# Optimization experiments

Measured on AMD Instinct MI355X. Metric: run time of the kernel, lower is better.

Reference implementation:

```python
import jax, jax.numpy as jnp
import numpy as np

N = 50000
E = 800000
IN_DIM = 256
H1, D1 = 4, 128   # layer1: 4 heads x 128 = 512 concat
H2, D2 = 1, 256   # layer2: 1 head x 256
NEG_SLOPE = 0.2


def setup_inputs() -> dict:
    key = jax.random.key(0)
    ks = jax.random.split(key, 12)
    feat = jax.random.normal(ks[0], (N, IN_DIM), dtype=jnp.float32)
    src1 = jax.random.randint(ks[1], (E,), 0, N)
    dst1 = jax.random.randint(ks[2], (E,), 0, N)
    src2 = jax.random.randint(ks[3], (E,), 0, N)
    dst2 = jax.random.randint(ks[4], (E,), 0, N)
    s1 = 1.0 / np.sqrt(IN_DIM)
    s2 = 1.0 / np.sqrt(H1 * D1)
    W1 = jax.random.normal(ks[5], (IN_DIM, H1 * D1), dtype=jnp.float32) * s1
    al1 = jax.random.normal(ks[6], (H1, D1), dtype=jnp.float32) * s1
    ar1 = jax.random.normal(ks[7], (H1, D1), dtype=jnp.float32) * s1
    W2 = jax.random.normal(ks[8], (H1 * D1, H2 * D2), dtype=jnp.float32) * s2
    al2 = jax.random.normal(ks[9], (H2, D2), dtype=jnp.float32) * s2
    ar2 = jax.random.normal(ks[10], (H2, D2), dtype=jnp.float32) * s2
    return {"feat": feat, "src1": src1, "dst1": dst1, "src2": src2,
            "dst2": dst2, "W1": W1, "al1": al1, "ar1": ar1,
            "W2": W2, "al2": al2, "ar2": ar2}


def gat_layer(x, W, al, ar, src, dst, heads):
    n = x.shape[0]
    h = (x @ W).reshape(n, heads, -1)               # [N,H,D]
    el = jnp.einsum('nhd,hd->nh', h, al)            # attention left term
    er = jnp.einsum('nhd,hd->nh', h, ar)            # attention right term
    e = jax.nn.leaky_relu(el[src] + er[dst], NEG_SLOPE)   # [E,H]
    # segment softmax over edges grouped by destination node
    m = jax.ops.segment_max(e, dst, num_segments=n)
    m = jax.lax.stop_gradient(jnp.where(jnp.isfinite(m), m, 0.0))
    ee = jnp.exp(e - m[dst])
    s = jax.ops.segment_sum(ee, dst, num_segments=n)
    alpha = ee / (s[dst] + 1e-9)                    # [E,H]
    msg = h[src] * alpha[:, :, None]                # [E,H,D]
    return jax.ops.segment_sum(msg, dst, num_segments=n)  # [N,H,D]


def reference(feat, src1, dst1, src2, dst2, W1, al1, ar1, W2, al2, ar2):
    h1 = gat_layer(feat, W1, al1, ar1, src1, dst1, H1)      # [N,4,128]
    h1 = jax.nn.elu(h1.reshape(N, H1 * D1))                 # concat heads + act
    z = gat_layer(h1, W2, al2, ar2, src2, dst2, H2)         # [N,1,256]
    return z.reshape(N, D2)                                 # no act on last layer
```

## Files before the change

kernel.cpp:

```cpp
#include <hip/hip_runtime.h>
#include <stdint.h>

#define NN 50000
#define EE 800000
#define IND 256
#define HD1 512
#define D2C 256

#define NB1 782
#define NB  (2 * NB1)
#define CH  16384
#define WGN ((2 * EE + CH - 1) / CH)
#define TOT (NB * WGN)
#define SB2 ((TOT + 255) / 256)

#define Q_SCALE 21.166666f
#define Q_INV   0.047244094f

typedef float f32x4 __attribute__((ext_vector_type(4)));
typedef __bf16 bf16x8 __attribute__((ext_vector_type(8)));

__device__ inline float bf2f(unsigned int u) {
    union { unsigned int i; float f; } c; c.i = u << 16; return c.f;
}
__device__ inline unsigned int f2bf(float f) {
    union { float f; unsigned int i; } c; c.f = f;
    unsigned int x = c.i;
    return (x + 0x7FFFu + ((x >> 16) & 1u)) >> 16;
}
__device__ inline float loadf(const void* p, int idx, int isbf) {
    return isbf ? bf2f(((const unsigned short*)p)[idx]) : ((const float*)p)[idx];
}
__device__ inline unsigned int f2q8(float v) {
    float t = fminf(fmaxf(v * Q_SCALE, -127.f), 127.f);
    int q = (int)rintf(t);
    return (unsigned int)q & 0xFFu;
}
__device__ inline void unpack8_q8(uint2 q, float* o) {
    o[0] = (float)(int)(signed char)(q.x & 0xFFu);
    o[1] = (float)(int)(signed char)((q.x >> 8) & 0xFFu);
    o[2] = (float)(int)(signed char)((q.x >> 16) & 0xFFu);
    o[3] = (float)(int)(signed char)(q.x >> 24);
    o[4] = (float)(int)(signed char)(q.y & 0xFFu);
    o[5] = (float)(int)(signed char)((q.y >> 8) & 0xFFu);
    o[6] = (float)(int)(signed char)((q.y >> 16) & 0xFFu);
    o[7] = (float)(int)(signed char)(q.y >> 24);
}
__device__ inline void glds16(const unsigned short* g, unsigned short* lds_base) {
    __builtin_amdgcn_global_load_lds(
        (const __attribute__((address_space(1))) void*)g,
        (__attribute__((address_space(3))) void*)lds_base, 16, 0, 0);
}

__global__ void probe_k(const unsigned int* __restrict__ w, int* __restrict__ flag) {
    __shared__ int red[256];
    int t = threadIdx.x;
    int ok = 0;
    for (int i = t; i < 4096; i += 256) {
        unsigned int v = w[i];
        unsigned int e0 = (v >> 7) & 0xffu;
        unsigned int e1 = (v >> 23) & 0xffu;
        ok += (e0 <= 133u) + (e1 <= 133u);
    }
    red[t] = ok;
    __syncthreads();
    for (int s = 128; s > 0; s >>= 1) {
        if (t < s) red[t] += red[t + s];
        __syncthreads();
    }
    if (t == 0) *flag = (red[0] >= 7782) ? 1 : 0;
}

__global__ __launch_bounds__(256) void convert_k(
    const void* __restrict__ in, const int* __restrict__ flagp,
    unsigned short* __restrict__ out)
{
    int isbf = (*flagp != 0);
    size_t i = ((size_t)blockIdx.x * 256 + threadIdx.x) * 8;
    if (i >= (size_t)NN * IND) return;
    if (isbf) {
        *(uint4*)(out + i) = *(const uint4*)((const unsigned short*)in + i);
    } else {
        const float* f = (const float*)in + i;
        f32x4 p0 = *(const f32x4*)f;
        f32x4 p1 = *(const f32x4*)(f + 4);
        uint4 va;
        va.x = f2bf(p0.x) | (f2bf(p0.y) << 16);
        va.y = f2bf(p0.z) | (f2bf(p0.w) << 16);
        va.z = f2bf(p1.x) | (f2bf(p1.y) << 16);
        va.w = f2bf(p1.z) | (f2bf(p1.w) << 16);
        *(uint4*)(out + i) = va;
    }
}

__global__ __launch_bounds__(256) void gemm_bt(
    const unsigned short* __restrict__ A, const int* __restrict__ flagp,
    const unsigned short* __restrict__ BT,
    void* __restrict__ C, int c_q8,
    int M, int K, int Nc,
    const void* __restrict__ al, const void* __restrict__ ar,
    float* __restrict__ el, float* __restrict__ er, int eler_mode)
{
    __shared__ unsigned short Als[128 * 32];
    __shared__ unsigned short Bls[128 * 32];
    __shared__ float elp[128];
    __shared__ float erp[128];
    int isbf = (*flagp != 0);
    int tid  = threadIdx.x;
    int wave = tid >> 6;
    int lane = tid & 63;
    int wr = (wave >> 1) * 64;
    int wc = (wave & 1) * 64;
    int m0 = blockIdx.x * 128;
    int n0 = blockIdx.y * 128;
    if (tid < 128) { elp[tid] = 0.f; erp[tid] = 0.f; }
    f32x4 acc[4][4];
#pragma unroll
    for (int i = 0; i < 4; i++)
#pragma unroll
        for (int j = 0; j < 4; j++) acc[i][j] = (f32x4){0.f, 0.f, 0.f, 0.f};
    int frow = lane & 15;
    int kg = (lane >> 4) * 8;
    int srow = lane >> 2;
    int scol = (lane & 3) * 8;
    for (int kt = 0; kt < K; kt += 32) {
#pragma unroll
        for (int q = 0; q < 2; ++q) {
            int chunk = wave + q * 4;
            int r = chunk * 16 + srow;
            int gm = m0 + r; if (gm >= M) gm = M - 1;
            glds16(A + (size_t)gm * K + kt + scol, Als + chunk * 512);
            glds16(BT + (size_t)(n0 + r) * K + kt + scol, Bls + chunk * 512);
        }
        __syncthreads();
        bf16x8 af[4], bfr[4];
#pragma unroll
        for (int i = 0; i < 4; i++)
            af[i] = __builtin_bit_cast(bf16x8, *(const uint4*)(Als + (wr + i * 16 + frow) * 32 + kg));
#pragma unroll
        for (int j = 0; j < 4; j++)
            bfr[j] = __builtin_bit_cast(bf16x8, *(const uint4*)(Bls + (wc + j * 16 + frow) * 32 + kg));
#pragma unroll
        for (int i = 0; i < 4; i++)
#pragma unroll
            for (int j = 0; j < 4; j++)
                acc[i][j] = __builtin_amdgcn_mfma_f32_16x16x32_bf16(af[i], bfr[j], acc[i][j], 0, 0, 0);
        __syncthreads();
    }
    int nb = n0 + wc + frow;
    int mb = m0 + wr + (lane >> 4) * 4;
#pragma unroll
    for (int i = 0; i < 4; i++) {
#pragma unroll
        for (int j = 0; j < 4; j++) {
            int n = nb + j * 16;
#pragma unroll
            for (int r = 0; r < 4; r++) {
                int m = mb + i * 16 + r;
                if (m < M) {
                    if (c_q8)
                        ((unsigned char*)C)[(size_t)m * Nc + n] = (unsigned char)f2q8(acc[i][j][r]);
                    else
                        ((unsigned short*)C)[(size_t)m * Nc + n] = (unsigned short)f2bf(acc[i][j][r]);
                }
            }
        }
    }
    float alv[4], arv[4];
#pragma unroll
    for (int j = 0; j < 4; j++) {
        int c = n0 + wc + frow + j * 16;
        alv[j] = loadf(al, c, isbf);
        arv[j] = loadf(ar, c, isbf);
    }
#pragma unroll
    for (int i = 0; i < 4; i++) {
#pragma unroll
        for (int r = 0; r < 4; r++) {
            float pe = 0.f, pr = 0.f;
#pragma unroll
            for (int j = 0; j < 4; j++) {
                pe += acc[i][j][r] * alv[j];
                pr += acc[i][j][r] * arv[j];
            }
#pragma unroll
            for (int o = 1; o < 16; o <<= 1) {
                pe += __shfl_xor(pe, o);
                pr += __shfl_xor(pr, o);
            }
            if ((lane & 15) == 0) {
                int row = wr + (lane >> 4) * 4 + i * 16 + r;
                atomicAdd(&elp[row], pe);
                atomicAdd(&erp[row], pr);
            }
        }
    }
    __syncthreads();
    if (tid < 128) {
        int m = m0 + tid;
        if (m < M) {
            if (eler_mode == 1) {
                el[m * 4 + blockIdx.y] = elp[tid];
                er[m * 4 + blockIdx.y] = erp[tid];
            } else {
                atomicAdd(&el[m], elp[tid]);
                atomicAdd(&er[m], erp[tid]);
            }
        }
    }
}

__global__ void transpose_k(const void* __restrict__ in, const int* __restrict__ flagp,
                            unsigned short* __restrict__ out, int R, int C) {
    int isbf = (*flagp != 0);
    int idx = blockIdx.x * blockDim.x + threadIdx.x;
    if (idx < R * C) {
        int i = idx / C, j = idx - i * C;
        unsigned short v = isbf ? ((const unsigned short*)in)[idx]
                                : (unsigned short)f2bf(((const float*)in)[idx]);
        out[j * R + i] = v;
    }
}

__global__ __launch_bounds__(256) void binA_k(
    const int* __restrict__ dst1, const int* __restrict__ dst2,
    int* __restrict__ hist)
{
    __shared__ int lh[NB];
    int t = threadIdx.x, w = blockIdx.x;
    for (int b = t; b < NB; b += 256) lh[b] = 0;
    __syncthreads();
    int base = w * CH;
    for (int k = 0; k < CH; k += 256) {
        int i = base + k + t;
        if (i < 2 * EE) {
            int d, lay;
            if (i < EE) { d = dst1[i]; lay = 0; }
            else        { d = dst2[i - EE]; lay = 1; }
            d = ((unsigned)d < (unsigned)NN) ? d : 0;
            atomicAdd(&lh[lay * NB1 + (d >> 6)], 1);
        }
    }
    __syncthreads();
    for (int b = t; b < NB; b += 256) hist[b * WGN + w] = lh[b];
}
__global__ void scan_a(int* __restrict__ hist, int* __restrict__ bsum) {
    __shared__ int sdata[256];
    int t = threadIdx.x;
    int g = blockIdx.x * 256 + t;
    int v = (g < TOT) ? hist[g] : 0;
    sdata[t] = v;
    __syncthreads();
    for (int o = 1; o < 256; o <<= 1) {
        int x = (t >= o) ? sdata[t - o] : 0;
        __syncthreads();
        sdata[t] += x;
        __syncthreads();
    }
    if (g < TOT) hist[g] = sdata[t] - v;
    if (t == 255) bsum[blockIdx.x] = sdata[255];
}
__global__ void scan_b(const int* __restrict__ bsum, int* __restrict__ boff) {
    __shared__ int sdata[1024];
    int t = threadIdx.x;
    int v = (t < SB2) ? bsum[t] : 0;
    sdata[t] = v;
    __syncthreads();
    for (int o = 1; o < 1024; o <<= 1) {
        int x = (t >= o) ? sdata[t - o] : 0;
        __syncthreads();
        sdata[t] += x;
        __syncthreads();
    }
    boff[t] = sdata[t] - v;
}
__global__ void scan_c(int* __restrict__ hist, const int* __restrict__ boff) {
    int g = blockIdx.x * 256 + threadIdx.x;
    if (g < TOT) hist[g] += boff[blockIdx.x];
}
__global__ __launch_bounds__(256) void binC_k(
    const int* __restrict__ src1, const int* __restrict__ dst1,
    const int* __restrict__ src2, const int* __restrict__ dst2,
    const int* __restrict__ base_g, unsigned int* __restrict__ bucketed)
{
    __shared__ int cur[NB];
    int t = threadIdx.x, w = blockIdx.x;
    for (int b = t; b < NB; b += 256) cur[b] = base_g[b * WGN + w];
    __syncthreads();
    int base = w * CH;
    for (int k = 0; k < CH; k += 256) {
        int i = base + k + t;
        if (i < 2 * EE) {
            int d, s, lay;
            if (i < EE) { d = dst1[i]; s = src1[i]; lay = 0; }
            else        { d = dst2[i - EE]; s = src2[i - EE]; lay = 1; }
            d = ((unsigned)d < (unsigned)NN) ? d : 0;
            s = ((unsigned)s < (unsigned)NN) ? s : 0;
            int b = lay * NB1 + (d >> 6);
            int p = atomicAdd(&cur[b], 1);
            bucketed[p] = (unsigned)s | ((unsigned)(d & 63) << 16);
        }
    }
}
__global__ __launch_bounds__(256) void binD_k(
    const int* __restrict__ base_g, const unsigned int* __restrict__ bucketed,
    int* __restrict__ csr, int* __restrict__ row_ptr)
{
    __shared__ int cnt[64];
    __shared__ int off[64];
    __shared__ int cur[64];
    int b = blockIdx.x, t = threadIdx.x;
    int s = base_g[b * WGN];
    int e = (b + 1 < NB) ? base_g[(b + 1) * WGN] : (2 * EE);
    int lay = (b >= NB1) ? 1 : 0;
    int b0 = b - lay * NB1;
    if (t < 64) cnt[t] = 0;
    __syncthreads();
    for (int i = s + t; i < e; i += 256)
        atomicAdd(&cnt[bucketed[i] >> 16], 1);
    __syncthreads();
    if (t == 0) {
        int run = s;
        for (int j = 0; j < 64; j++) { off[j] = run; run += cnt[j]; }
    }
    __syncthreads();
    if (t < 64) {
        int node = b0 * 64 + t;
        if (node < NN) row_ptr[lay * NN + node] = off[t];
        cur[t] = off[t];
    }
    __syncthreads();
    for (int i = s + t; i < e; i += 256) {
        unsigned v = bucketed[i];
        int p = atomicAdd(&cur[v >> 16], 1);
        csr[p] = (int)(v & 0xFFFFu);
    }
    if (b == NB - 1 && t == 0) row_ptr[2 * NN] = e;
}

__global__ __launch_bounds__(256) void agg1_k(
    const unsigned char* __restrict__ h1,
    const float* __restrict__ el, const float* __restrict__ er,
    const int* __restrict__ row_ptr, const int* __restrict__ csr,
    unsigned short* __restrict__ x2)
{
    int wv = (blockIdx.x * blockDim.x + threadIdx.x) >> 6;
    int lane = threadIdx.x & 63;
    if (wv >= NN) return;
    int h = lane >> 4;
    float erv = er[wv * 4 + h];
    int e0 = row_ptr[wv], e1 = row_ptr[wv + 1];
    float l = 0.f;
    float acc[8];
#pragma unroll
    for (int j = 0; j < 8; j++) acc[j] = 0.f;
    int e = e0;
    for (; e + 1 < e1; e += 2) {
        int s0 = csr[e];
        int s1 = csr[e + 1];
        s0 = ((unsigned)s0 < (unsigned)NN) ? s0 : 0;
        s1 = ((unsigned)s1 < (unsigned)NN) ? s1 : 0;
        float ev0 = el[s0 * 4 + h] + erv;
        float ev1 = el[s1 * 4 + h] + erv;
        ev0 = (ev0 > 0.f) ? ev0 : 0.2f * ev0;
        ev1 = (ev1 > 0.f) ? ev1 : 0.2f * ev1;
        float w0 = __expf(fminf(ev0, 80.f));
        float w1 = __expf(fminf(ev1, 80.f));
        uint2 p0 = *(const uint2*)(h1 + (size_t)s0 * HD1 + lane * 8);
        uint2 p1 = *(const uint2*)(h1 + (size_t)s1 * HD1 + lane * 8);
        float f0[8], f1[8];
        unpack8_q8(p0, f0);
        unpack8_q8(p1, f1);
        l += w0 + w1;
        float w0s = w0 * Q_INV, w1s = w1 * Q_INV;
#pragma unroll
        for (int j = 0; j < 8; j++) acc[j] += w0s * f0[j] + w1s * f1[j];
    }
    if (e < e1) {
        int s = csr[e];
        s = ((unsigned)s < (unsigned)NN) ? s : 0;
        float ev = el[s * 4 + h] + erv;
        ev = (ev > 0.f) ? ev : 0.2f * ev;
        float wgt = __expf(fminf(ev, 80.f));
        l += wgt;
        float hf[8];
        unpack8_q8(*(const uint2*)(h1 + (size_t)s * HD1 + lane * 8), hf);
        float ws = wgt * Q_INV;
#pragma unroll
        for (int j = 0; j < 8; j++) acc[j] += ws * hf[j];
    }
    float inv = 1.f / (l + 1e-9f);
    unsigned int o[4];
#pragma unroll
    for (int j = 0; j < 4; j++) {
        float v0 = acc[2 * j] * inv;
        float v1 = acc[2 * j + 1] * inv;
        v0 = (v0 > 0.f) ? v0 : (__expf(v0) - 1.f);
        v1 = (v1 > 0.f) ? v1 : (__expf(v1) - 1.f);
        o[j] = f2bf(v0) | (f2bf(v1) << 16);
    }
    *(uint4*)(x2 + (size_t)wv * HD1 + lane * 8) = make_uint4(o[0], o[1], o[2], o[3]);
}

__global__ __launch_bounds__(256) void agg2_k(
    const unsigned short* __restrict__ h2,
    const float* __restrict__ el, const float* __restrict__ er,
    const int* __restrict__ row_ptr, const int* __restrict__ csr,
    void* __restrict__ outv, const int* __restrict__ flagp)
{
    int isbf = (*flagp != 0);
    int wv = (blockIdx.x * blockDim.x + threadIdx.x) >> 6;
    int lane = threadIdx.x & 63;
    if (wv >= NN) return;
    float erv = er[wv];
    int e0 = row_ptr[NN + wv], e1 = row_ptr[NN + wv + 1];
    float l = 0.f;
    float a0 = 0.f, a1 = 0.f, a2 = 0.f, a3 = 0.f;
    int e = e0;
    for (; e + 1 < e1; e += 2) {
        int s0 = csr[e];
        int s1 = csr[e + 1];
        s0 = ((unsigned)s0 < (unsigned)NN) ? s0 : 0;
        s1 = ((unsigned)s1 < (unsigned)NN) ? s1 : 0;
        float ev0 = el[s0] + erv;
        float ev1 = el[s1] + erv;
        ev0 = (ev0 > 0.f) ? ev0 : 0.2f * ev0;
        ev1 = (ev1 > 0.f) ? ev1 : 0.2f * ev1;
        float w0 = __expf(fminf(ev0, 80.f));
        float w1 = __expf(fminf(ev1, 80.f));
        uint2 t0 = *(const uint2*)(h2 + (size_t)s0 * D2C + lane * 4);
        uint2 t1 = *(const uint2*)(h2 + (size_t)s1 * D2C + lane * 4);
        l += w0 + w1;
        a0 += w0 * bf2f(t0.x & 0xffffu) + w1 * bf2f(t1.x & 0xffffu);
        a1 += w0 * bf2f(t0.x >> 16)     + w1 * bf2f(t1.x >> 16);
        a2 += w0 * bf2f(t0.y & 0xffffu) + w1 * bf2f(t1.y & 0xffffu);
        a3 += w0 * bf2f(t0.y >> 16)     + w1 * bf2f(t1.y >> 16);
    }
    if (e < e1) {
        int s = csr[e];
        s = ((unsigned)s < (unsigned)NN) ? s : 0;
        float ev = el[s] + erv;
        ev = (ev > 0.f) ? ev : 0.2f * ev;
        float wgt = __expf(fminf(ev, 80.f));
        l += wgt;
        uint2 t = *(const uint2*)(h2 + (size_t)s * D2C + lane * 4);
        a0 += wgt * bf2f(t.x & 0xffffu);
        a1 += wgt * bf2f(t.x >> 16);
        a2 += wgt * bf2f(t.y & 0xffffu);
        a3 += wgt * bf2f(t.y >> 16);
    }
    float inv = 1.f / (l + 1e-9f);
    float v0 = a0 * inv, v1 = a1 * inv, v2 = a2 * inv, v3 = a3 * inv;
    if (isbf) {
        uint2 o;
        o.x = f2bf(v0) | (f2bf(v1) << 16);
        o.y = f2bf(v2) | (f2bf(v3) << 16);
        *(uint2*)((unsigned short*)outv + (size_t)wv * D2C + lane * 4) = o;
    } else {
        f32x4 o = (f32x4){v0, v1, v2, v3};
        *(f32x4*)((float*)outv + (size_t)wv * D2C + lane * 4) = o;
    }
}

extern "C" void kernel_launch(void* const* d_in, const int* in_sizes, int n_in,
                              void* d_out, int out_size, void* d_ws, size_t ws_size,
                              hipStream_t stream) {
    const void* feat = d_in[0];
    const int* src1 = (const int*)d_in[1];
    const int* dst1 = (const int*)d_in[2];
    const int* src2 = (const int*)d_in[3];
    const int* dst2 = (const int*)d_in[4];
    const void* W1  = d_in[5];
    const void* al1 = d_in[6];
    const void* ar1 = d_in[7];
    const void* W2  = d_in[8];
    const void* al2 = d_in[9];
    const void* ar2 = d_in[10];

    uint8_t* w = (uint8_t*)d_ws;
    auto alloc = [&](size_t bytes) -> void* {
        void* p = (void*)w;
        w += (bytes + 255) & ~(size_t)255;
        return p;
    };
    int* flag    = (int*)alloc(256);
    float* el    = (float*)alloc((size_t)NN * 4 * 4);
    float* er    = (float*)alloc((size_t)NN * 4 * 4);
    unsigned short* W1T = (unsigned short*)alloc((size_t)IND * HD1 * 2);
    unsigned short* W2T = (unsigned short*)alloc((size_t)HD1 * D2C * 2);
    int* hist    = (int*)alloc((size_t)TOT * 4);
    int* bsum    = (int*)alloc(1024 * 4);
    int* boff    = (int*)alloc(1024 * 4);
    unsigned int* bucketed = (unsigned int*)alloc((size_t)2 * EE * 4);
    int* csr     = (int*)alloc((size_t)2 * EE * 4);
    int* row_ptr = (int*)alloc((size_t)(2 * NN + 1) * 4);
    unsigned char* h1 = (unsigned char*)alloc((size_t)NN * HD1);
    unsigned short* x2 = (unsigned short*)alloc((size_t)NN * HD1 * 2);
    unsigned short* h2 = (unsigned short*)h1;
    unsigned short* featb = x2;

    probe_k<<<1, 256, 0, stream>>>((const unsigned int*)feat, flag);
    convert_k<<<(NN * IND / 8 + 255) / 256, 256, 0, stream>>>(feat, flag, featb);
    transpose_k<<<(IND * HD1 + 255) / 256, 256, 0, stream>>>(W1, flag, W1T, IND, HD1);
    transpose_k<<<(HD1 * D2C + 255) / 256, 256, 0, stream>>>(W2, flag, W2T, HD1, D2C);

    binA_k<<<WGN, 256, 0, stream>>>(dst1, dst2, hist);
    scan_a<<<SB2, 256, 0, stream>>>(hist, bsum);
    scan_b<<<1, 1024, 0, stream>>>(bsum, boff);
    scan_c<<<SB2, 256, 0, stream>>>(hist, boff);
    binC_k<<<WGN, 256, 0, stream>>>(src1, dst1, src2, dst2, hist, bucketed);
    binD_k<<<NB, 256, 0, stream>>>(hist, bucketed, csr, row_ptr);

    gemm_bt<<<dim3((NN + 127) / 128, HD1 / 128), 256, 0, stream>>>(
        featb, flag, W1T, h1, 1, NN, IND, HD1, al1, ar1, el, er, 1);
    agg1_k<<<(NN + 3) / 4, 256, 0, stream>>>(h1, el, er, row_ptr, csr, x2);

    hipMemsetAsync(el, 0, (size_t)NN * 4, stream);
    hipMemsetAsync(er, 0, (size_t)NN * 4, stream);
    gemm_bt<<<dim3((NN + 127) / 128, D2C / 128), 256, 0, stream>>>(
        x2, flag, W2T, (void*)h2, 0, NN, HD1, D2C, al2, ar2, el, er, 2);
    agg2_k<<<(NN + 3) / 4, 256, 0, stream>>>(h2, el, er, row_ptr, csr, d_out, flag);
}
```

Baseline: 455.9 us.

## Precompute per-edge attention weights in separate kernels and use offset uint8 quantization

Adds wgt1_k/wgt2_k kernels that compute the leaky-relu/exp attention weight once per edge (and head), storing dst in the upper 16 bits of CSR entries so the weight kernels can find er. The aggregation kernels then read precomputed weights instead of gathering el and evaluating exp redundantly across the 16 lanes sharing a head. Layer-1 features are quantized as uint8 with a +128 offset, and the bias is removed at the end using the weight sum. This adds two launches and extra per-edge weight buffers in global memory.

```diff
diff --git a/kernel.cpp b/kernel.cpp
--- a/kernel.cpp
+++ b/kernel.cpp
@@ -33,18 +33,18 @@
 }
 __device__ inline unsigned int f2q8(float v) {
     float t = fminf(fmaxf(v * Q_SCALE, -127.f), 127.f);
-    int q = (int)rintf(t);
+    int q = (int)rintf(t) + 128;
     return (unsigned int)q & 0xFFu;
 }
-__device__ inline void unpack8_q8(uint2 q, float* o) {
-    o[0] = (float)(int)(signed char)(q.x & 0xFFu);
-    o[1] = (float)(int)(signed char)((q.x >> 8) & 0xFFu);
-    o[2] = (float)(int)(signed char)((q.x >> 16) & 0xFFu);
-    o[3] = (float)(int)(signed char)(q.x >> 24);
-    o[4] = (float)(int)(signed char)(q.y & 0xFFu);
-    o[5] = (float)(int)(signed char)((q.y >> 8) & 0xFFu);
-    o[6] = (float)(int)(signed char)((q.y >> 16) & 0xFFu);
-    o[7] = (float)(int)(signed char)(q.y >> 24);
+__device__ inline void unpack8_u8(uint2 q, float* o) {
+    o[0] = (float)(q.x & 0xFFu);
+    o[1] = (float)((q.x >> 8) & 0xFFu);
+    o[2] = (float)((q.x >> 16) & 0xFFu);
+    o[3] = (float)(q.x >> 24);
+    o[4] = (float)(q.y & 0xFFu);
+    o[5] = (float)((q.y >> 8) & 0xFFu);
+    o[6] = (float)((q.y >> 16) & 0xFFu);
+    o[7] = (float)(q.y >> 24);
 }
 __device__ inline void glds16(const unsigned short* g, unsigned short* lds_base) {
     __builtin_amdgcn_global_load_lds(
@@ -333,14 +333,47 @@
     for (int i = s + t; i < e; i += 256) {
         unsigned v = bucketed[i];
         int p = atomicAdd(&cur[v >> 16], 1);
-        csr[p] = (int)(v & 0xFFFFu);
+        unsigned node = (unsigned)(b0 * 64) + (v >> 16);
+        csr[p] = (int)((v & 0xFFFFu) | (node << 16));
     }
     if (b == NB - 1 && t == 0) row_ptr[2 * NN] = e;
+}
+
+__global__ __launch_bounds__(256) void wgt1_k(
+    const int* __restrict__ csr, const float* __restrict__ el,
+    const float* __restrict__ er, float* __restrict__ w)
+{
+    int idx = blockIdx.x * 256 + threadIdx.x;
+    if (idx >= EE * 4) return;
+    int p = idx >> 2, h = idx & 3;
+    unsigned c = (unsigned)csr[p];
+    int s = (int)(c & 0xFFFFu);
+    int d = (int)(c >> 16);
+    s = ((unsigned)s < (unsigned)NN) ? s : 0;
+    d = ((unsigned)d < (unsigned)NN) ? d : 0;
+    float ev = el[s * 4 + h] + er[d * 4 + h];
+    ev = (ev > 0.f) ? ev : 0.2f * ev;
+    w[idx] = __expf(fminf(ev, 80.f));
+}
+__global__ __launch_bounds__(256) void wgt2_k(
+    const int* __restrict__ csr, const float* __restrict__ el,
+    const float* __restrict__ er, float* __restrict__ w)
+{
+    int p = blockIdx.x * 256 + threadIdx.x;
+    if (p >= EE) return;
+    unsigned c = (unsigned)csr[EE + p];
+    int s = (int)(c & 0xFFFFu);
+    int d = (int)(c >> 16);
+    s = ((unsigned)s < (unsigned)NN) ? s : 0;
+    d = ((unsigned)d < (unsigned)NN) ? d : 0;
+    float ev = el[s] + er[d];
+    ev = (ev > 0.f) ? ev : 0.2f * ev;
+    w[p] = __expf(fminf(ev, 80.f));
 }
 
 __global__ __launch_bounds__(256) void agg1_k(
     const unsigned char* __restrict__ h1,
-    const float* __restrict__ el, const float* __restrict__ er,
+    const float* __restrict__ wgt,
     const int* __restrict__ row_ptr, const int* __restrict__ csr,
     unsigned short* __restrict__ x2)
 {
@@ -348,7 +381,6 @@
     int lane = threadIdx.x & 63;
     if (wv >= NN) return;
     int h = lane >> 4;
-    float erv = er[wv * 4 + h];
     int e0 = row_ptr[wv], e1 = row_ptr[wv + 1];
     float l = 0.f;
     float acc[8];
@@ -356,45 +388,39 @@
     for (int j = 0; j < 8; j++) acc[j] = 0.f;
     int e = e0;
     for (; e + 1 < e1; e += 2) {
-        int s0 = csr[e];
-        int s1 = csr[e + 1];
+        int s0 = csr[e] & 0xFFFF;
+        int s1 = csr[e + 1] & 0xFFFF;
         s0 = ((unsigned)s0 < (unsigned)NN) ? s0 : 0;
         s1 = ((unsigned)s1 < (unsigned)NN) ? s1 : 0;
-        float ev0 = el[s0 * 4 + h] + erv;
-        float ev1 = el[s1 * 4 + h] + erv;
-        ev0 = (ev0 > 0.f) ? ev0 : 0.2f * ev0;
-        ev1 = (ev1 > 0.f) ? ev1 : 0.2f * ev1;
-        float w0 = __expf(fminf(ev0, 80.f));
-        float w1 = __expf(fminf(ev1, 80.f));
+        float w0 = wgt[e * 4 + h];
+        float w1 = wgt[(e + 1) * 4 + h];
         uint2 p0 = *(const uint2*)(h1 + (size_t)s0 * HD1 + lane * 8);
         uint2 p1 = *(const uint2*)(h1 + (size_t)s1 * HD1 + lane * 8);
         float f0[8], f1[8];
-        unpack8_q8(p0, f0);
-        unpack8_q8(p1, f1);
+        unpack8_u8(p0, f0);
+        unpack8_u8(p1, f1);
         l += w0 + w1;
-        float w0s = w0 * Q_INV, w1s = w1 * Q_INV;
-#pragma unroll
-        for (int j = 0; j < 8; j++) acc[j] += w0s * f0[j] + w1s * f1[j];
+#pragma unroll
+        for (int j = 0; j < 8; j++) acc[j] += w0 * f0[j] + w1 * f1[j];
     }
     if (e < e1) {
-        int s = csr[e];
+        int s = csr[e] & 0xFFFF;
         s = ((unsigned)s < (unsigned)NN) ? s : 0;
-        float ev = el[s * 4 + h] + erv;
-        ev = (ev > 0.f) ? ev : 0.2f * ev;
-        float wgt = __expf(fminf(ev, 80.f));
-        l += wgt;
+        float w0 = wgt[e * 4 + h];
+        l += w0;
         float hf[8];
-        unpack8_q8(*(const uint2*)(h1 + (size_t)s * HD1 + lane * 8), hf);
-        float ws = wgt * Q_INV;
-#pragma unroll
-        for (int j = 0; j < 8; j++) acc[j] += ws * hf[j];
+        unpack8_u8(*(const uint2*)(h1 + (size_t)s * HD1 + lane * 8), hf);
+#pragma unroll
+        for (int j = 0; j < 8; j++) acc[j] += w0 * hf[j];
     }
     float inv = 1.f / (l + 1e-9f);
+    float sc = Q_INV * inv;
+    float bias = 128.f * l;
     unsigned int o[4];
 #pragma unroll
     for (int j = 0; j < 4; j++) {
-        float v0 = acc[2 * j] * inv;
-        float v1 = acc[2 * j + 1] * inv;
+        float v0 = (acc[2 * j] - bias) * sc;
+        float v1 = (acc[2 * j + 1] - bias) * sc;
         v0 = (v0 > 0.f) ? v0 : (__expf(v0) - 1.f);
         v1 = (v1 > 0.f) ? v1 : (__expf(v1) - 1.f);
         o[j] = f2bf(v0) | (f2bf(v1) << 16);
@@ -404,7 +430,7 @@
 
 __global__ __launch_bounds__(256) void agg2_k(
     const unsigned short* __restrict__ h2,
-    const float* __restrict__ el, const float* __restrict__ er,
+    const float* __restrict__ wgt,
     const int* __restrict__ row_ptr, const int* __restrict__ csr,
     void* __restrict__ outv, const int* __restrict__ flagp)
 {
@@ -412,22 +438,17 @@
     int wv = (blockIdx.x * blockDim.x + threadIdx.x) >> 6;
     int lane = threadIdx.x & 63;
     if (wv >= NN) return;
-    float erv = er[wv];
     int e0 = row_ptr[NN + wv], e1 = row_ptr[NN + wv + 1];
     float l = 0.f;
     float a0 = 0.f, a1 = 0.f, a2 = 0.f, a3 = 0.f;
     int e = e0;
     for (; e + 1 < e1; e += 2) {
-        int s0 = csr[e];
-        int s1 = csr[e + 1];
+        int s0 = csr[e] & 0xFFFF;
+        int s1 = csr[e + 1] & 0xFFFF;
         s0 = ((unsigned)s0 < (unsigned)NN) ? s0 : 0;
         s1 = ((unsigned)s1 < (unsigned)NN) ? s1 : 0;
-        float ev0 = el[s0] + erv;
-        float ev1 = el[s1] + erv;
-        ev0 = (ev0 > 0.f) ? ev0 : 0.2f * ev0;
-        ev1 = (ev1 > 0.f) ? ev1 : 0.2f * ev1;
-        float w0 = __expf(fminf(ev0, 80.f));
-        float w1 = __expf(fminf(ev1, 80.f));
+        float w0 = wgt[e - EE];
+        float w1 = wgt[e + 1 - EE];
         uint2 t0 = *(const uint2*)(h2 + (size_t)s0 * D2C + lane * 4);
         uint2 t1 = *(const uint2*)(h2 + (size_t)s1 * D2C + lane * 4);
         l += w0 + w1;
@@ -437,17 +458,15 @@
         a3 += w0 * bf2f(t0.y >> 16)     + w1 * bf2f(t1.y >> 16);
     }
     if (e < e1) {
-        int s = csr[e];
+        int s = csr[e] & 0xFFFF;
         s = ((unsigned)s < (unsigned)NN) ? s : 0;
-        float ev = el[s] + erv;
-        ev = (ev > 0.f) ? ev : 0.2f * ev;
-        float wgt = __expf(fminf(ev, 80.f));
-        l += wgt;
+        float w0 = wgt[e - EE];
+        l += w0;
         uint2 t = *(const uint2*)(h2 + (size_t)s * D2C + lane * 4);
-        a0 += wgt * bf2f(t.x & 0xffffu);
-        a1 += wgt * bf2f(t.x >> 16);
-        a2 += wgt * bf2f(t.y & 0xffffu);
-        a3 += wgt * bf2f(t.y >> 16);
+        a0 += w0 * bf2f(t.x & 0xffffu);
+        a1 += w0 * bf2f(t.x >> 16);
+        a2 += w0 * bf2f(t.y & 0xffffu);
+        a3 += w0 * bf2f(t.y >> 16);
     }
     float inv = 1.f / (l + 1e-9f);
     float v0 = a0 * inv, v1 = a1 * inv, v2 = a2 * inv, v3 = a3 * inv;
@@ -496,8 +515,10 @@
     int* row_ptr = (int*)alloc((size_t)(2 * NN + 1) * 4);
     unsigned char* h1 = (unsigned char*)alloc((size_t)NN * HD1);
     unsigned short* x2 = (unsigned short*)alloc((size_t)NN * HD1 * 2);
+    float* w1e   = (float*)alloc((size_t)EE * 4 * 4);
     unsigned short* h2 = (unsigned short*)h1;
     unsigned short* featb = x2;
+    float* w2e   = (float*)bucketed;
 
     probe_k<<<1, 256, 0, stream>>>((const unsigned int*)feat, flag);
     convert_k<<<(NN * IND / 8 + 255) / 256, 256, 0, stream>>>(feat, flag, featb);
@@ -513,11 +534,13 @@
 
     gemm_bt<<<dim3((NN + 127) / 128, HD1 / 128), 256, 0, stream>>>(
         featb, flag, W1T, h1, 1, NN, IND, HD1, al1, ar1, el, er, 1);
-    agg1_k<<<(NN + 3) / 4, 256, 0, stream>>>(h1, el, er, row_ptr, csr, x2);
+    wgt1_k<<<(EE * 4 + 255) / 256, 256, 0, stream>>>(csr, el, er, w1e);
+    agg1_k<<<(NN + 3) / 4, 256, 0, stream>>>(h1, w1e, row_ptr, csr, x2);
 
     hipMemsetAsync(el, 0, (size_t)NN * 4, stream);
     hipMemsetAsync(er, 0, (size_t)NN * 4, stream);
     gemm_bt<<<dim3((NN + 127) / 128, D2C / 128), 256, 0, stream>>>(
         x2, flag, W2T, (void*)h2, 0, NN, HD1, D2C, al2, ar2, el, er, 2);
-    agg2_k<<<(NN + 3) / 4, 256, 0, stream>>>(h2, el, er, row_ptr, csr, d_out, flag);
-}
+    wgt2_k<<<(EE + 255) / 256, 256, 0, stream>>>(csr, el, er, w2e);
+    agg2_k<<<(NN + 3) / 4, 256, 0, stream>>>(h2, w2e, row_ptr, csr, d_out, flag);
+}
```

New measurement: 466.7 us. 1.02x slower.
